# Performance work log

Hardware: AMD Instinct MI355X
Metric: run time of the kernel (lower is better)

## Reference

```python
import jax, jax.numpy as jnp
import numpy as np

N = 100000
E = 1600000
D_IN = 128
H = 128


def _param(key, shape, scale=0.05):
    return jax.random.normal(key, shape, dtype=jnp.float32) * scale


def setup_inputs() -> dict:
    key = jax.random.key(0)
    ks = jax.random.split(key, 24)
    inp = {
        'x': jax.random.normal(ks[0], (N, D_IN), dtype=jnp.float32),
        'edge_index': jax.random.randint(ks[1], (2, E), 0, N, dtype=jnp.int64),
        'h1': jax.random.normal(ks[2], (N, H), dtype=jnp.float32),
        'h2': jax.random.normal(ks[3], (N, H), dtype=jnp.float32),
        'h3': jax.random.normal(ks[4], (N, H), dtype=jnp.float32),
        # GCNConv params (PyG: lin weight applied as x @ W, W: [in, out] here)
        'gcn1_w': _param(ks[5], (D_IN, H)),
        'gcn1_b': jnp.zeros((H,), jnp.float32),
        'gcn2_w': _param(ks[6], (H, H)),
        'gcn2_b': jnp.zeros((H,), jnp.float32),
    }
    # torch.nn.GRUCell params: weight_ih [3H, in], weight_hh [3H, H], biases [3H]
    for i, kw in zip((1, 2, 3), (ks[7], ks[10], ks[13])):
        k1, k2, k3 = jax.random.split(kw, 3)
        inp[f'gru{i}_wih'] = _param(k1, (3 * H, H))
        inp[f'gru{i}_whh'] = _param(k2, (3 * H, H))
        inp[f'gru{i}_bih'] = _param(k3, (3 * H,))
        inp[f'gru{i}_bhh'] = jnp.zeros((3 * H,), jnp.float32)
    return inp


def gcn_conv(x, src, dst, w, b):
    """PyG GCNConv: D^-1/2 (A+I) D^-1/2 X W + b (symmetric norm, self-loops)."""
    xw = x @ w  # [N, H]
    ones = jnp.ones((src.shape[0],), xw.dtype)
    # degree including self-loop
    deg = jax.ops.segment_sum(ones, dst, num_segments=N) + 1.0
    dinv = jax.lax.rsqrt(deg)
    norm = dinv[src] * dinv[dst]  # [E]
    agg = jax.ops.segment_sum(xw[src] * norm[:, None], dst, num_segments=N)
    # self-loop contribution: norm = dinv[i]*dinv[i] = 1/deg[i]
    return agg + xw / deg[:, None] + b


def gru_cell(x, h, w_ih, w_hh, b_ih, b_hh):
    gi = x @ w_ih.T + b_ih  # [N, 3H]
    gh = h @ w_hh.T + b_hh
    i_r, i_z, i_n = jnp.split(gi, 3, axis=-1)
    h_r, h_z, h_n = jnp.split(gh, 3, axis=-1)
    r = jax.nn.sigmoid(i_r + h_r)
    z = jax.nn.sigmoid(i_z + h_z)
    n = jnp.tanh(i_n + r * h_n)
    return (1.0 - z) * n + z * h


def reference(x, edge_index, h1, h2, h3,
              gcn1_w, gcn1_b, gcn2_w, gcn2_b,
              gru1_wih, gru1_whh, gru1_bih, gru1_bhh,
              gru2_wih, gru2_whh, gru2_bih, gru2_bhh,
              gru3_wih, gru3_whh, gru3_bih, gru3_bhh):
    src, dst = edge_index[0], edge_index[1]
    x = jax.nn.relu(gcn_conv(x, src, dst, gcn1_w, gcn1_b))
    # dropout is identity at eval
    x = jax.nn.relu(gcn_conv(x, src, dst, gcn2_w, gcn2_b))
    h1n = gru_cell(x, h1, gru1_wih, gru1_whh, gru1_bih, gru1_bhh)
    h2n = gru_cell(h1n, h2, gru2_wih, gru2_whh, gru2_bih, gru2_bhh)
    h3n = gru_cell(h2n, h3, gru3_wih, gru3_whh, gru3_bih, gru3_bhh)
    return (h1n, h2n, h3n)
```

## Files before the change

### kernel.cpp

```cpp
#include <hip/hip_runtime.h>
#include <hip/hip_bf16.h>

#define DH 128
#define SCB 1024
#define NCHUNK 256
#define LROW 136

typedef __attribute__((ext_vector_type(8))) short short8_t;
typedef __attribute__((ext_vector_type(4))) float f32x4;

static __device__ __forceinline__ short f2bf(float f) {
    union { float f; unsigned u; } v; v.f = f;
    unsigned r = v.u + 0x7fffu + ((v.u >> 16) & 1u);
    return (short)(r >> 16);
}

static __device__ __forceinline__ float bf2f(unsigned short b) {
    union { unsigned u; float f; } v; v.u = ((unsigned)b) << 16;
    return v.f;
}

static __device__ __forceinline__ short8_t cvt8(const float* p) {
    float4 a0 = *(const float4*)p;
    float4 a1 = *(const float4*)(p + 4);
    short8_t t;
    t[0] = f2bf(a0.x); t[1] = f2bf(a0.y); t[2] = f2bf(a0.z); t[3] = f2bf(a0.w);
    t[4] = f2bf(a1.x); t[5] = f2bf(a1.y); t[6] = f2bf(a1.z); t[7] = f2bf(a1.w);
    return t;
}

static __device__ __forceinline__ float sigm(float x) {
    return __builtin_amdgcn_rcpf(1.f + __expf(-x));
}
static __device__ __forceinline__ float tanh_f(float x) {
    return 1.f - 2.f * __builtin_amdgcn_rcpf(__expf(2.f * x) + 1.f);
}

__global__ __launch_bounds__(256) void deg2_k(const int* __restrict__ ei, int E,
                                              unsigned* __restrict__ cnt, int span, int chunkE) {
    int r = blockIdx.x & 7;
    int c = blockIdx.x >> 3;
    int lo = r * span, hi = lo + span;
    long long e0 = (long long)c * chunkE;
    long long e1 = e0 + chunkE; if (e1 > E) e1 = E;
    for (long long e = e0 + threadIdx.x; e < e1; e += 256) {
        int d = ei[E + e];
        if (d >= lo && d < hi) atomicAdd(&cnt[d], 1u);
    }
}

__global__ __launch_bounds__(256) void scan1_k(const unsigned* __restrict__ cnt, int N,
                                               int* __restrict__ offs, unsigned* __restrict__ bsum) {
    __shared__ unsigned s[256];
    int t = threadIdx.x;
    int i0 = blockIdx.x * SCB + t * 4;
    unsigned v0 = (i0 + 0 < N) ? cnt[i0 + 0] : 0u;
    unsigned v1 = (i0 + 1 < N) ? cnt[i0 + 1] : 0u;
    unsigned v2 = (i0 + 2 < N) ? cnt[i0 + 2] : 0u;
    unsigned v3 = (i0 + 3 < N) ? cnt[i0 + 3] : 0u;
    unsigned ts = v0 + v1 + v2 + v3;
    s[t] = ts;
    __syncthreads();
    for (int off = 1; off < 256; off <<= 1) {
        unsigned u = (t >= off) ? s[t - off] : 0u;
        __syncthreads();
        s[t] += u;
        __syncthreads();
    }
    unsigned ex = s[t] - ts;
    if (i0 + 0 < N) offs[i0 + 0] = (int)ex;
    if (i0 + 1 < N) offs[i0 + 1] = (int)(ex + v0);
    if (i0 + 2 < N) offs[i0 + 2] = (int)(ex + v0 + v1);
    if (i0 + 3 < N) offs[i0 + 3] = (int)(ex + v0 + v1 + v2);
    if (t == 255) bsum[blockIdx.x] = s[255];
}

__global__ __launch_bounds__(1024) void scan2_k(unsigned* __restrict__ bsum, int B) {
    __shared__ unsigned s[1024];
    int t = threadIdx.x;
    unsigned v = (t < B) ? bsum[t] : 0u;
    s[t] = v;
    __syncthreads();
    for (int off = 1; off < 1024; off <<= 1) {
        unsigned u = (t >= off) ? s[t - off] : 0u;
        __syncthreads();
        s[t] += u;
        __syncthreads();
    }
    if (t < B) bsum[t] = s[t] - v;
    if (t == 0) bsum[B] = s[1023];
}

__global__ void scan3_k(int* __restrict__ offs, int* __restrict__ cur,
                        float* __restrict__ dinv, const unsigned* __restrict__ cnt,
                        const unsigned* __restrict__ bsum, int N, int B) {
    int i = blockIdx.x * 256 + threadIdx.x;
    if (i < N) {
        int v = offs[i] + (int)bsum[i >> 10];
        offs[i] = v;
        cur[i] = v;
        dinv[i] = rsqrtf((float)cnt[i] + 1.0f);
    }
    if (i == 0) offs[N] = (int)bsum[B];
}

__global__ __launch_bounds__(256) void fill2_k(const int* __restrict__ ei, int E,
                                               int* __restrict__ cur, int* __restrict__ csr_src,
                                               int span, int chunkE) {
    int r = blockIdx.x & 7;
    int c = blockIdx.x >> 3;
    int lo = r * span, hi = lo + span;
    long long e0 = (long long)c * chunkE;
    long long e1 = e0 + chunkE; if (e1 > E) e1 = E;
    for (long long e = e0 + threadIdx.x; e < e1; e += 256) {
        int d = ei[E + e];
        if (d >= lo && d < hi) {
            int pos = atomicAdd(&cur[d], 1);
            csr_src[pos] = ei[e];
        }
    }
}

__global__ void f2bf6_k(const float* __restrict__ s0, const float* __restrict__ s1,
                        const float* __restrict__ s2, const float* __restrict__ s3,
                        const float* __restrict__ s4, const float* __restrict__ s5,
                        short* __restrict__ dst, int WN) {
    int i = blockIdx.x * 256 + threadIdx.x;
    if (i >= 6 * WN) return;
    int b = i / WN, r = i - b * WN;
    const float* srcs[6] = {s0, s1, s2, s3, s4, s5};
    dst[i] = f2bf(srcs[b][r]);
}

__global__ void transpose_bf2_k(const float* __restrict__ sa, const float* __restrict__ sb,
                                short* __restrict__ da, short* __restrict__ db) {
    int i = blockIdx.x * 256 + threadIdx.x;
    int m = i >> 14;
    int j = i & 16383;
    int c = j >> 7, k = j & 127;
    const float* s = m ? sb : sa;
    short* d = m ? db : da;
    d[j] = f2bf(s[k * DH + c]);
}

__global__ __launch_bounds__(256, 4) void gemm_mfma_k(const float* __restrict__ A,
                                                      const short* __restrict__ Wt,
                                                      const float* __restrict__ dinv,
                                                      short* __restrict__ C, int N) {
    int tid = threadIdx.x;
    int wave = tid >> 6, lane = tid & 63;
    int lr = lane & 15, kg = lane >> 4;

    int row0 = blockIdx.x * 128 + wave * 32;
    int ar0 = min(row0 + lr, N - 1);
    int ar1 = min(row0 + 16 + lr, N - 1);
    const float* a0p = A + (size_t)ar0 * DH;
    const float* a1p = A + (size_t)ar1 * DH;
    short8_t af[2][4];
#pragma unroll
    for (int ks = 0; ks < 4; ks++) {
        af[0][ks] = cvt8(a0p + ks * 32 + kg * 8);
        af[1][ks] = cvt8(a1p + ks * 32 + kg * 8);
    }

    float di0[4], di1[4];
#pragma unroll
    for (int j = 0; j < 4; j++) {
        di0[j] = dinv[min(row0 + kg * 4 + j, N - 1)];
        di1[j] = dinv[min(row0 + 16 + kg * 4 + j, N - 1)];
    }

    short8_t bt[3][4];
#define GLOADW(slot, t) { \
    const short* wp = Wt + (size_t)((t) * 16 + lr) * DH + kg * 8; \
    bt[slot][0] = *(const short8_t*)(wp); \
    bt[slot][1] = *(const short8_t*)(wp + 32); \
    bt[slot][2] = *(const short8_t*)(wp + 64); \
    bt[slot][3] = *(const short8_t*)(wp + 96); }

    GLOADW(0, 0)
    GLOADW(1, 1)
#pragma unroll
    for (int t = 0; t < 8; t++) {
        if (t < 6) GLOADW((t + 2) % 3, t + 2)
        f32x4 acc0 = {0.f, 0.f, 0.f, 0.f};
        f32x4 acc1 = {0.f, 0.f, 0.f, 0.f};
#pragma unroll
        for (int ks = 0; ks < 4; ks++) {
            acc0 = __builtin_amdgcn_mfma_f32_16x16x32_bf16(af[0][ks], bt[t % 3][ks], acc0, 0, 0, 0);
            acc1 = __builtin_amdgcn_mfma_f32_16x16x32_bf16(af[1][ks], bt[t % 3][ks], acc1, 0, 0, 0);
        }
        int col = t * 16 + lr;
#pragma unroll
        for (int j = 0; j < 4; j++) {
            int g0 = row0 + kg * 4 + j;
            int g1 = row0 + 16 + kg * 4 + j;
            if (g0 < N) C[(size_t)g0 * DH + col] = f2bf(acc0[j] * di0[j]);
            if (g1 < N) C[(size_t)g1 * DH + col] = f2bf(acc1[j] * di1[j]);
        }
    }
#undef GLOADW
}

__global__ __launch_bounds__(256) void gather_k(const int* __restrict__ csr_src,
                                                const int* __restrict__ offs,
                                                const float* __restrict__ dinv,
                                                const unsigned* __restrict__ xws,
                                                const float* __restrict__ bias,
                                                float* __restrict__ dest, int N) {
    int wid = blockIdx.x * 4 + (threadIdx.x >> 6);
    if (wid >= N) return;
    int lane = threadIdx.x & 63;
    int j = offs[wid];
    int end = offs[wid + 1];
    float dd = dinv[wid];

    unsigned xv = xws[(size_t)wid * 64 + lane];
    float ax = bf2f((unsigned short)(xv & 0xffffu));
    float ay = bf2f((unsigned short)(xv >> 16));

#define ACC(w) { ax += bf2f((unsigned short)((w) & 0xffffu)); \
                 ay += bf2f((unsigned short)((w) >> 16)); }

    if (j + 4 <= end) {
        int a0 = csr_src[j], a1 = csr_src[j + 1], a2 = csr_src[j + 2], a3 = csr_src[j + 3];
        j += 4;
        for (; j + 4 <= end; j += 4) {
            unsigned w0 = xws[(size_t)a0 * 64 + lane];
            unsigned w1 = xws[(size_t)a1 * 64 + lane];
            unsigned w2 = xws[(size_t)a2 * 64 + lane];
            unsigned w3 = xws[(size_t)a3 * 64 + lane];
            a0 = csr_src[j]; a1 = csr_src[j + 1]; a2 = csr_src[j + 2]; a3 = csr_src[j + 3];
            ACC(w0) ACC(w1) ACC(w2) ACC(w3)
        }
        unsigned w0 = xws[(size_t)a0 * 64 + lane];
        unsigned w1 = xws[(size_t)a1 * 64 + lane];
        unsigned w2 = xws[(size_t)a2 * 64 + lane];
        unsigned w3 = xws[(size_t)a3 * 64 + lane];
        ACC(w0) ACC(w1) ACC(w2) ACC(w3)
    }
    for (; j < end; ++j) {
        unsigned w = xws[(size_t)csr_src[j] * 64 + lane];
        ACC(w)
    }
#undef ACC

    float2 b2 = ((const float2*)bias)[lane];
    float ox = fmaxf(fmaf(dd, ax, b2.x), 0.f);
    float oy = fmaxf(fmaf(dd, ay, b2.y), 0.f);
    float2 o; o.x = ox; o.y = oy;
    ((float2*)dest)[(size_t)wid * 64 + lane] = o;
}

__global__ __launch_bounds__(512, 1) void gru3_mfma_k(
        const float* __restrict__ X, const float* __restrict__ H1,
        const float* __restrict__ H2, const float* __restrict__ H3,
        const short* __restrict__ w1i, const short* __restrict__ w1h,
        const short* __restrict__ w2i, const short* __restrict__ w2h,
        const short* __restrict__ w3i, const short* __restrict__ w3h,
        const float* __restrict__ bi1, const float* __restrict__ bh1,
        const float* __restrict__ bi2, const float* __restrict__ bh2,
        const float* __restrict__ bi3, const float* __restrict__ bh3,
        float* __restrict__ o1, float* __restrict__ o2, float* __restrict__ o3,
        int N) {
    __shared__ short lds[4][64 * LROW];
    int tid = threadIdx.x;
    int row0 = blockIdx.x * 64;
    int wave = tid >> 6, lane = tid & 63;
    int lr = lane & 15, kg = lane >> 4;
    int c0 = wave * 16;

    const short* wihs[3] = {w1i, w2i, w3i};
    const short* whhs[3] = {w1h, w2h, w3h};
    const float* bihs[3] = {bi1, bi2, bi3};
    const float* bhhs[3] = {bh1, bh2, bh3};
    float* outs[3] = {o1, o2, o3};

    short8_t bw[3][4], bu[3][4];
#define WLOADALL(wih_, whh_) { \
    _Pragma("unroll") \
    for (int g = 0; g < 3; g++) { \
        const short* wi = (wih_) + (size_t)(g * DH + c0 + lr) * DH + kg * 8; \
        const short* wh = (whh_) + (size_t)(g * DH + c0 + lr) * DH + kg * 8; \
        _Pragma("unroll") \
        for (int ks = 0; ks < 4; ks++) { \
            bw[g][ks] = *(const short8_t*)(wi + ks * 32); \
            bu[g][ks] = *(const short8_t*)(wh + ks * 32); \
        } \
    } }

    {
        const float* mats[4] = {X, H1, H2, H3};
        int mat = tid >> 7;
        int rr = (tid & 127) >> 1;
        int q = tid & 1;
        int grow = min(row0 + rr, N - 1);
        const float* src = mats[mat] + (size_t)grow * DH + q * 64;
        char* dst = (char*)&lds[mat][rr * LROW] + q * 128;
#pragma unroll
        for (int j = 0; j < 8; j++) {
            short8_t v = cvt8(src + j * 8);
            *(short8_t*)(dst + j * 16) = v;
        }
    }
    WLOADALL(w1i, w1h)
    __syncthreads();

    int gcol = c0 + lr;
    int colb = gcol * 2;

#pragma unroll
    for (int cell = 0; cell < 3; cell++) {
        const short* hslot = lds[cell + 1];
        f32x4 aR[4], aZ[4], aI[4], aH[4];
#pragma unroll
        for (int rt = 0; rt < 4; rt++) {
            aR[rt] = (f32x4){0,0,0,0}; aZ[rt] = (f32x4){0,0,0,0};
            aI[rt] = (f32x4){0,0,0,0}; aH[rt] = (f32x4){0,0,0,0};
        }
#pragma unroll
        for (int rt = 0; rt < 4; rt++) {
            int r = rt * 16 + lr;
            const char* xrow = (const char*)&lds[0][r * LROW];
            const char* hrow = (const char*)&hslot[r * LROW];
            short8_t xa[4], ha[4];
#pragma unroll
            for (int ks = 0; ks < 4; ks++) {
                int boff = ks * 64 + kg * 16;
                xa[ks] = *(const short8_t*)(xrow + boff);
                ha[ks] = *(const short8_t*)(hrow + boff);
            }
#pragma unroll
            for (int ks = 0; ks < 4; ks++) {
                aR[rt] = __builtin_amdgcn_mfma_f32_16x16x32_bf16(xa[ks], bw[0][ks], aR[rt], 0, 0, 0);
                aR[rt] = __builtin_amdgcn_mfma_f32_16x16x32_bf16(ha[ks], bu[0][ks], aR[rt], 0, 0, 0);
                aZ[rt] = __builtin_amdgcn_mfma_f32_16x16x32_bf16(xa[ks], bw[1][ks], aZ[rt], 0, 0, 0);
                aZ[rt] = __builtin_amdgcn_mfma_f32_16x16x32_bf16(ha[ks], bu[1][ks], aZ[rt], 0, 0, 0);
                aI[rt] = __builtin_amdgcn_mfma_f32_16x16x32_bf16(xa[ks], bw[2][ks], aI[rt], 0, 0, 0);
                aH[rt] = __builtin_amdgcn_mfma_f32_16x16x32_bf16(ha[ks], bu[2][ks], aH[rt], 0, 0, 0);
            }
        }

        const float* bih = bihs[cell];
        const float* bhh = bhhs[cell];
        float br = bih[gcol], bz = bih[DH + gcol], bn = bih[2 * DH + gcol];
        float cr = bhh[gcol], cz = bhh[DH + gcol], cn = bhh[2 * DH + gcol];
        float* outp = outs[cell];
        short hb[4][4];
#pragma unroll
        for (int rt = 0; rt < 4; rt++) {
#pragma unroll
            for (int j = 0; j < 4; j++) {
                int r = rt * 16 + kg * 4 + j;
                float hv = bf2f(*(const unsigned short*)((const char*)&hslot[r * LROW] + colb));
                float rr = sigm(aR[rt][j] + br + cr);
                float zz = sigm(aZ[rt][j] + bz + cz);
                float nn = tanh_f(aI[rt][j] + bn + rr * (aH[rt][j] + cn));
                float ov = (1.f - zz) * nn + zz * hv;
                int grow = row0 + r;
                if (grow < N) outp[(size_t)grow * DH + gcol] = ov;
                hb[rt][j] = f2bf(ov);
            }
        }

        if (cell < 2) {
            WLOADALL(wihs[cell + 1], whhs[cell + 1])
        }

        __syncthreads();

        if (cell < 2) {
#pragma unroll
            for (int rt = 0; rt < 4; rt++) {
#pragma unroll
                for (int j = 0; j < 4; j++) {
                    int r = rt * 16 + kg * 4 + j;
                    *(short*)((char*)&lds[0][r * LROW] + colb) = hb[rt][j];
                }
            }
            __syncthreads();
        }
    }
#undef WLOADALL
}

extern "C" void kernel_launch(void* const* d_in, const int* in_sizes, int n_in,
                              void* d_out, int out_size, void* d_ws, size_t ws_size,
                              hipStream_t stream) {
    const float* x    = (const float*)d_in[0];
    const int*   ei   = (const int*)d_in[1];
    const float* h1   = (const float*)d_in[2];
    const float* h2   = (const float*)d_in[3];
    const float* h3   = (const float*)d_in[4];
    const float* g1w  = (const float*)d_in[5];
    const float* g1b  = (const float*)d_in[6];
    const float* g2w  = (const float*)d_in[7];
    const float* g2b  = (const float*)d_in[8];
    const float* wih1 = (const float*)d_in[9];
    const float* whh1 = (const float*)d_in[10];
    const float* bih1 = (const float*)d_in[11];
    const float* bhh1 = (const float*)d_in[12];
    const float* wih2 = (const float*)d_in[13];
    const float* whh2 = (const float*)d_in[14];
    const float* bih2 = (const float*)d_in[15];
    const float* bhh2 = (const float*)d_in[16];
    const float* wih3 = (const float*)d_in[17];
    const float* whh3 = (const float*)d_in[18];
    const float* bih3 = (const float*)d_in[19];
    const float* bhh3 = (const float*)d_in[20];

    int N = in_sizes[0] / DH;
    int E = in_sizes[1] / 2;
    int B = (N + SCB - 1) / SCB;
    int nstripes = (N + 127) / 128;
    int nblk64 = (N + 63) / 64;
    int span = (N + 7) / 8;
    int chunkE = (E + NCHUNK - 1) / NCHUNK;

    char* wsp = (char*)d_ws;
    auto alloc = [&](size_t bytes) -> char* {
        char* p = wsp;
        wsp += (bytes + 63) & ~(size_t)63;
        return p;
    };
    unsigned* cnt = (unsigned*)alloc((size_t)N * 4);
    int* offs     = (int*)alloc(((size_t)N + 1) * 4);
    int* cur      = (int*)alloc((size_t)N * 4);
    float* dinv   = (float*)alloc((size_t)N * 4);
    unsigned* bsum= (unsigned*)alloc(((size_t)B + 1) * 4);
    int* csr_src  = (int*)alloc((size_t)E * 4);
    short* xwb    = (short*)alloc((size_t)N * DH * 2);
    float* x2     = (float*)alloc((size_t)N * DH * 4);
    short* w1t    = (short*)alloc((size_t)DH * DH * 2);
    short* w2t    = (short*)alloc((size_t)DH * DH * 2);
    const int WN = 3 * DH * DH;
    short* wbAll  = (short*)alloc((size_t)6 * WN * 2);
    short* wb[6];
    for (int i = 0; i < 6; i++) wb[i] = wbAll + (size_t)i * WN;

    float* out  = (float*)d_out;
    float* h1n  = out;
    float* h2n  = out + (size_t)N * DH;
    float* h3n  = out + 2 * (size_t)N * DH;

    f2bf6_k<<<(6 * WN + 255) / 256, 256, 0, stream>>>(wih1, whh1, wih2, whh2, wih3, whh3, wbAll, WN);
    transpose_bf2_k<<<(2 * DH * DH + 255) / 256, 256, 0, stream>>>(g1w, g2w, w1t, w2t);

    hipMemsetAsync(cnt, 0, (size_t)N * 4, stream);
    deg2_k<<<8 * NCHUNK, 256, 0, stream>>>(ei, E, cnt, span, chunkE);
    scan1_k<<<B, 256, 0, stream>>>(cnt, N, offs, bsum);
    scan2_k<<<1, 1024, 0, stream>>>(bsum, B);
    scan3_k<<<(N + 255) / 256, 256, 0, stream>>>(offs, cur, dinv, cnt, bsum, N, B);
    fill2_k<<<8 * NCHUNK, 256, 0, stream>>>(ei, E, cur, csr_src, span, chunkE);

    int gblocks = (N + 3) / 4;

    gemm_mfma_k<<<nstripes, 256, 0, stream>>>(x, w1t, dinv, xwb, N);
    gather_k<<<gblocks, 256, 0, stream>>>(csr_src, offs, dinv, (const unsigned*)xwb, g1b, x2, N);

    gemm_mfma_k<<<nstripes, 256, 0, stream>>>(x2, w2t, dinv, xwb, N);
    gather_k<<<gblocks, 256, 0, stream>>>(csr_src, offs, dinv, (const unsigned*)xwb, g2b, x2, N);

    gru3_mfma_k<<<nblk64, 512, 0, stream>>>(x2, h1, h2, h3,
                                            wb[0], wb[1], wb[2], wb[3], wb[4], wb[5],
                                            bih1, bhh1, bih2, bhh2, bih3, bhh3,
                                            h1n, h2n, h3n, N);
}
```

Baseline: 589.4 us.

## Store GCN intermediate features as FP8 and stream GRU hidden states per cell

The scaled XW features written by the GEMM are now encoded in a software e4m3-style FP8 format instead of bf16, which halves the bytes the edge-gather kernel pulls per neighbor. The gather decodes the FP8 values in software before accumulating. Separately, the GRU kernel shrinks its LDS from four to two tiles and loads the next cell's hidden state (H2/H3) from global memory while the current cell computes, which should raise occupancy. The FP8 path loses a lot of precision on the aggregated features and adds decode ALU work per element.

```diff
diff --git a/kernel.cpp b/kernel.cpp
--- a/kernel.cpp
+++ b/kernel.cpp
@@ -20,9 +20,40 @@
     return v.f;
 }
 
+static __device__ __forceinline__ unsigned char fp8enc(float f) {
+    union { float f; unsigned u; } v; v.f = f;
+    unsigned s = v.u >> 31;
+    unsigned mag = v.u & 0x7fffffffu;
+    if (mag >= 0x43E00000u) return (unsigned char)((s << 7) | 0x7E);
+    unsigned e = mag >> 23;
+    if (e < 121u) {
+        int q = (int)rintf(fabsf(f) * 512.0f);
+        return (unsigned char)((s << 7) | (unsigned)q);
+    }
+    unsigned r = mag + 0x7FFFFu + ((mag >> 20) & 1u);
+    unsigned e2 = r >> 23, m2 = (r >> 20) & 7u;
+    if (e2 > 135u || (e2 == 135u && m2 == 7u)) return (unsigned char)((s << 7) | 0x7E);
+    return (unsigned char)((s << 7) | ((e2 - 120u) << 3) | m2);
+}
+
+static __device__ __forceinline__ float fp8dec(unsigned b) {
+    unsigned s = b >> 7, E = (b >> 3) & 0xFu, m = b & 7u;
+    union { unsigned u; float f; } v;
+    v.u = (s << 31) | ((E + 120u) << 23) | (m << 20);
+    float sub = (s ? -1.953125e-3f : 1.953125e-3f) * (float)m;
+    return E ? v.f : sub;
+}
+
 static __device__ __forceinline__ short8_t cvt8(const float* p) {
     float4 a0 = *(const float4*)p;
     float4 a1 = *(const float4*)(p + 4);
+    short8_t t;
+    t[0] = f2bf(a0.x); t[1] = f2bf(a0.y); t[2] = f2bf(a0.z); t[3] = f2bf(a0.w);
+    t[4] = f2bf(a1.x); t[5] = f2bf(a1.y); t[6] = f2bf(a1.z); t[7] = f2bf(a1.w);
+    return t;
+}
+
+static __device__ __forceinline__ short8_t cvt8v(float4 a0, float4 a1) {
     short8_t t;
     t[0] = f2bf(a0.x); t[1] = f2bf(a0.y); t[2] = f2bf(a0.z); t[3] = f2bf(a0.w);
     t[4] = f2bf(a1.x); t[5] = f2bf(a1.y); t[6] = f2bf(a1.z); t[7] = f2bf(a1.w);
@@ -146,7 +177,7 @@
 __global__ __launch_bounds__(256, 4) void gemm_mfma_k(const float* __restrict__ A,
                                                       const short* __restrict__ Wt,
                                                       const float* __restrict__ dinv,
-                                                      short* __restrict__ C, int N) {
+                                                      unsigned char* __restrict__ C, int N) {
     int tid = threadIdx.x;
     int wave = tid >> 6, lane = tid & 63;
     int lr = lane & 15, kg = lane >> 4;
@@ -195,8 +226,8 @@
         for (int j = 0; j < 4; j++) {
             int g0 = row0 + kg * 4 + j;
             int g1 = row0 + 16 + kg * 4 + j;
-            if (g0 < N) C[(size_t)g0 * DH + col] = f2bf(acc0[j] * di0[j]);
-            if (g1 < N) C[(size_t)g1 * DH + col] = f2bf(acc1[j] * di1[j]);
+            if (g0 < N) C[(size_t)g0 * DH + col] = fp8enc(acc0[j] * di0[j]);
+            if (g1 < N) C[(size_t)g1 * DH + col] = fp8enc(acc1[j] * di1[j]);
         }
     }
 #undef GLOADW
@@ -205,7 +236,7 @@
 __global__ __launch_bounds__(256) void gather_k(const int* __restrict__ csr_src,
                                                 const int* __restrict__ offs,
                                                 const float* __restrict__ dinv,
-                                                const unsigned* __restrict__ xws,
+                                                const unsigned short* __restrict__ xq2,
                                                 const float* __restrict__ bias,
                                                 float* __restrict__ dest, int N) {
     int wid = blockIdx.x * 4 + (threadIdx.x >> 6);
@@ -215,32 +246,31 @@
     int end = offs[wid + 1];
     float dd = dinv[wid];
 
-    unsigned xv = xws[(size_t)wid * 64 + lane];
-    float ax = bf2f((unsigned short)(xv & 0xffffu));
-    float ay = bf2f((unsigned short)(xv >> 16));
-
-#define ACC(w) { ax += bf2f((unsigned short)((w) & 0xffffu)); \
-                 ay += bf2f((unsigned short)((w) >> 16)); }
+    unsigned xv = xq2[(size_t)wid * 64 + lane];
+    float ax = fp8dec(xv & 0xffu);
+    float ay = fp8dec(xv >> 8);
+
+#define ACC(w) { ax += fp8dec((w) & 0xffu); ay += fp8dec((w) >> 8); }
 
     if (j + 4 <= end) {
         int a0 = csr_src[j], a1 = csr_src[j + 1], a2 = csr_src[j + 2], a3 = csr_src[j + 3];
         j += 4;
         for (; j + 4 <= end; j += 4) {
-            unsigned w0 = xws[(size_t)a0 * 64 + lane];
-            unsigned w1 = xws[(size_t)a1 * 64 + lane];
-            unsigned w2 = xws[(size_t)a2 * 64 + lane];
-            unsigned w3 = xws[(size_t)a3 * 64 + lane];
+            unsigned w0 = xq2[(size_t)a0 * 64 + lane];
+            unsigned w1 = xq2[(size_t)a1 * 64 + lane];
+            unsigned w2 = xq2[(size_t)a2 * 64 + lane];
+            unsigned w3 = xq2[(size_t)a3 * 64 + lane];
             a0 = csr_src[j]; a1 = csr_src[j + 1]; a2 = csr_src[j + 2]; a3 = csr_src[j + 3];
             ACC(w0) ACC(w1) ACC(w2) ACC(w3)
         }
-        unsigned w0 = xws[(size_t)a0 * 64 + lane];
-        unsigned w1 = xws[(size_t)a1 * 64 + lane];
-        unsigned w2 = xws[(size_t)a2 * 64 + lane];
-        unsigned w3 = xws[(size_t)a3 * 64 + lane];
+        unsigned w0 = xq2[(size_t)a0 * 64 + lane];
+        unsigned w1 = xq2[(size_t)a1 * 64 + lane];
+        unsigned w2 = xq2[(size_t)a2 * 64 + lane];
+        unsigned w3 = xq2[(size_t)a3 * 64 + lane];
         ACC(w0) ACC(w1) ACC(w2) ACC(w3)
     }
     for (; j < end; ++j) {
-        unsigned w = xws[(size_t)csr_src[j] * 64 + lane];
+        unsigned w = xq2[(size_t)csr_src[j] * 64 + lane];
         ACC(w)
     }
 #undef ACC
@@ -263,7 +293,7 @@
         const float* __restrict__ bi3, const float* __restrict__ bh3,
         float* __restrict__ o1, float* __restrict__ o2, float* __restrict__ o3,
         int N) {
-    __shared__ short lds[4][64 * LROW];
+    __shared__ short lds[2][64 * LROW];
     int tid = threadIdx.x;
     int row0 = blockIdx.x * 64;
     int wave = tid >> 6, lane = tid & 63;
@@ -289,29 +319,30 @@
         } \
     } }
 
+    WLOADALL(w1i, w1h)
+
     {
-        const float* mats[4] = {X, H1, H2, H3};
-        int mat = tid >> 7;
-        int rr = (tid & 127) >> 1;
-        int q = tid & 1;
-        int grow = min(row0 + rr, N - 1);
-        const float* src = mats[mat] + (size_t)grow * DH + q * 64;
-        char* dst = (char*)&lds[mat][rr * LROW] + q * 128;
-#pragma unroll
-        for (int j = 0; j < 8; j++) {
+        int mat = tid >> 8;
+        int r = (tid & 255) >> 2;
+        int q = tid & 3;
+        int grow = min(row0 + r, N - 1);
+        const float* src = (mat ? H1 : X) + (size_t)grow * DH + q * 32;
+        char* dst = (char*)&lds[mat][r * LROW] + q * 64;
+#pragma unroll
+        for (int j = 0; j < 4; j++) {
             short8_t v = cvt8(src + j * 8);
             *(short8_t*)(dst + j * 16) = v;
         }
     }
-    WLOADALL(w1i, w1h)
     __syncthreads();
 
     int gcol = c0 + lr;
     int colb = gcol * 2;
+    int srow = tid >> 3;
+    int sq = tid & 7;
 
 #pragma unroll
     for (int cell = 0; cell < 3; cell++) {
-        const short* hslot = lds[cell + 1];
         f32x4 aR[4], aZ[4], aI[4], aH[4];
 #pragma unroll
         for (int rt = 0; rt < 4; rt++) {
@@ -322,7 +353,7 @@
         for (int rt = 0; rt < 4; rt++) {
             int r = rt * 16 + lr;
             const char* xrow = (const char*)&lds[0][r * LROW];
-            const char* hrow = (const char*)&hslot[r * LROW];
+            const char* hrow = (const char*)&lds[1][r * LROW];
             short8_t xa[4], ha[4];
 #pragma unroll
             for (int ks = 0; ks < 4; ks++) {
@@ -341,6 +372,16 @@
             }
         }
 
+        float4 hs0, hs1, hs2, hs3;
+        if (cell < 2) {
+            int grow = min(row0 + srow, N - 1);
+            const float* src = (cell == 0 ? H2 : H3) + (size_t)grow * DH + sq * 16;
+            hs0 = *(const float4*)(src + 0);
+            hs1 = *(const float4*)(src + 4);
+            hs2 = *(const float4*)(src + 8);
+            hs3 = *(const float4*)(src + 12);
+        }
+
         const float* bih = bihs[cell];
         const float* bhh = bhhs[cell];
         float br = bih[gcol], bz = bih[DH + gcol], bn = bih[2 * DH + gcol];
@@ -352,7 +393,7 @@
 #pragma unroll
             for (int j = 0; j < 4; j++) {
                 int r = rt * 16 + kg * 4 + j;
-                float hv = bf2f(*(const unsigned short*)((const char*)&hslot[r * LROW] + colb));
+                float hv = bf2f(*(const unsigned short*)((const char*)&lds[1][r * LROW] + colb));
                 float rr = sigm(aR[rt][j] + br + cr);
                 float zz = sigm(aZ[rt][j] + bz + cz);
                 float nn = tanh_f(aI[rt][j] + bn + rr * (aH[rt][j] + cn));
@@ -377,6 +418,11 @@
                     int r = rt * 16 + kg * 4 + j;
                     *(short*)((char*)&lds[0][r * LROW] + colb) = hb[rt][j];
                 }
+            }
+            {
+                char* dst = (char*)&lds[1][srow * LROW] + sq * 32;
+                *(short8_t*)(dst) = cvt8v(hs0, hs1);
+                *(short8_t*)(dst + 16) = cvt8v(hs2, hs3);
             }
             __syncthreads();
         }
@@ -429,7 +475,7 @@
     float* dinv   = (float*)alloc((size_t)N * 4);
     unsigned* bsum= (unsigned*)alloc(((size_t)B + 1) * 4);
     int* csr_src  = (int*)alloc((size_t)E * 4);
-    short* xwb    = (short*)alloc((size_t)N * DH * 2);
+    unsigned char* xq = (unsigned char*)alloc((size_t)N * DH);
     float* x2     = (float*)alloc((size_t)N * DH * 4);
     short* w1t    = (short*)alloc((size_t)DH * DH * 2);
     short* w2t    = (short*)alloc((size_t)DH * DH * 2);
@@ -455,11 +501,11 @@
 
     int gblocks = (N + 3) / 4;
 
-    gemm_mfma_k<<<nstripes, 256, 0, stream>>>(x, w1t, dinv, xwb, N);
-    gather_k<<<gblocks, 256, 0, stream>>>(csr_src, offs, dinv, (const unsigned*)xwb, g1b, x2, N);
-
-    gemm_mfma_k<<<nstripes, 256, 0, stream>>>(x2, w2t, dinv, xwb, N);
-    gather_k<<<gblocks, 256, 0, stream>>>(csr_src, offs, dinv, (const unsigned*)xwb, g2b, x2, N);
+    gemm_mfma_k<<<nstripes, 256, 0, stream>>>(x, w1t, dinv, xq, N);
+    gather_k<<<gblocks, 256, 0, stream>>>(csr_src, offs, dinv, (const unsigned short*)xq, g1b, x2, N);
+
+    gemm_mfma_k<<<nstripes, 256, 0, stream>>>(x2, w2t, dinv, xq, N);
+    gather_k<<<gblocks, 256, 0, stream>>>(csr_src, offs, dinv, (const unsigned short*)xq, g2b, x2, N);
 
     gru3_mfma_k<<<nblk64, 512, 0, stream>>>(x2, h1, h2, h3,
                                             wb[0], wb[1], wb[2], wb[3], wb[4], wb[5],
```

Result: slower. 658.5 us (+11.7%).

## Halve GRU LDS footprint and prefetch next hidden state during current cell

Applied to the files above, without the earlier changes.

The fused three-cell GRU kernel now keeps only two LDS slots (input and current hidden) instead of four. H2 and H3 are loaded from global memory into registers while the current cell's epilogue runs, then converted to bf16 and written into the hidden slot after the barrier. Weight loads for the first cell are also issued before the initial tile staging. This cuts LDS use per block, which could allow more blocks per CU, and overlaps hidden-state loads with compute, at the cost of extra registers and less parallelism in the initial load.

```diff
diff --git a/kernel.cpp b/kernel.cpp
--- a/kernel.cpp
+++ b/kernel.cpp
@@ -23,6 +23,13 @@
 static __device__ __forceinline__ short8_t cvt8(const float* p) {
     float4 a0 = *(const float4*)p;
     float4 a1 = *(const float4*)(p + 4);
+    short8_t t;
+    t[0] = f2bf(a0.x); t[1] = f2bf(a0.y); t[2] = f2bf(a0.z); t[3] = f2bf(a0.w);
+    t[4] = f2bf(a1.x); t[5] = f2bf(a1.y); t[6] = f2bf(a1.z); t[7] = f2bf(a1.w);
+    return t;
+}
+
+static __device__ __forceinline__ short8_t cvt8v(float4 a0, float4 a1) {
     short8_t t;
     t[0] = f2bf(a0.x); t[1] = f2bf(a0.y); t[2] = f2bf(a0.z); t[3] = f2bf(a0.w);
     t[4] = f2bf(a1.x); t[5] = f2bf(a1.y); t[6] = f2bf(a1.z); t[7] = f2bf(a1.w);
@@ -263,7 +270,7 @@
         const float* __restrict__ bi3, const float* __restrict__ bh3,
         float* __restrict__ o1, float* __restrict__ o2, float* __restrict__ o3,
         int N) {
-    __shared__ short lds[4][64 * LROW];
+    __shared__ short lds[2][64 * LROW];
     int tid = threadIdx.x;
     int row0 = blockIdx.x * 64;
     int wave = tid >> 6, lane = tid & 63;
@@ -289,29 +296,30 @@
         } \
     } }
 
+    WLOADALL(w1i, w1h)
+
     {
-        const float* mats[4] = {X, H1, H2, H3};
-        int mat = tid >> 7;
-        int rr = (tid & 127) >> 1;
-        int q = tid & 1;
-        int grow = min(row0 + rr, N - 1);
-        const float* src = mats[mat] + (size_t)grow * DH + q * 64;
-        char* dst = (char*)&lds[mat][rr * LROW] + q * 128;
-#pragma unroll
-        for (int j = 0; j < 8; j++) {
+        int mat = tid >> 8;
+        int r = (tid & 255) >> 2;
+        int q = tid & 3;
+        int grow = min(row0 + r, N - 1);
+        const float* src = (mat ? H1 : X) + (size_t)grow * DH + q * 32;
+        char* dst = (char*)&lds[mat][r * LROW] + q * 64;
+#pragma unroll
+        for (int j = 0; j < 4; j++) {
             short8_t v = cvt8(src + j * 8);
             *(short8_t*)(dst + j * 16) = v;
         }
     }
-    WLOADALL(w1i, w1h)
     __syncthreads();
 
     int gcol = c0 + lr;
     int colb = gcol * 2;
+    int srow = tid >> 3;
+    int sq = tid & 7;
 
 #pragma unroll
     for (int cell = 0; cell < 3; cell++) {
-        const short* hslot = lds[cell + 1];
         f32x4 aR[4], aZ[4], aI[4], aH[4];
 #pragma unroll
         for (int rt = 0; rt < 4; rt++) {
@@ -322,7 +330,7 @@
         for (int rt = 0; rt < 4; rt++) {
             int r = rt * 16 + lr;
             const char* xrow = (const char*)&lds[0][r * LROW];
-            const char* hrow = (const char*)&hslot[r * LROW];
+            const char* hrow = (const char*)&lds[1][r * LROW];
             short8_t xa[4], ha[4];
 #pragma unroll
             for (int ks = 0; ks < 4; ks++) {
@@ -341,6 +349,16 @@
             }
         }
 
+        float4 hs0, hs1, hs2, hs3;
+        if (cell < 2) {
+            int grow = min(row0 + srow, N - 1);
+            const float* src = (cell == 0 ? H2 : H3) + (size_t)grow * DH + sq * 16;
+            hs0 = *(const float4*)(src + 0);
+            hs1 = *(const float4*)(src + 4);
+            hs2 = *(const float4*)(src + 8);
+            hs3 = *(const float4*)(src + 12);
+        }
+
         const float* bih = bihs[cell];
         const float* bhh = bhhs[cell];
         float br = bih[gcol], bz = bih[DH + gcol], bn = bih[2 * DH + gcol];
@@ -352,7 +370,7 @@
 #pragma unroll
             for (int j = 0; j < 4; j++) {
                 int r = rt * 16 + kg * 4 + j;
-                float hv = bf2f(*(const unsigned short*)((const char*)&hslot[r * LROW] + colb));
+                float hv = bf2f(*(const unsigned short*)((const char*)&lds[1][r * LROW] + colb));
                 float rr = sigm(aR[rt][j] + br + cr);
                 float zz = sigm(aZ[rt][j] + bz + cz);
                 float nn = tanh_f(aI[rt][j] + bn + rr * (aH[rt][j] + cn));
@@ -377,6 +395,11 @@
                     int r = rt * 16 + kg * 4 + j;
                     *(short*)((char*)&lds[0][r * LROW] + colb) = hb[rt][j];
                 }
+            }
+            {
+                char* dst = (char*)&lds[1][srow * LROW] + sq * 32;
+                *(short8_t*)(dst) = cvt8v(hs0, hs1);
+                *(short8_t*)(dst + 16) = cvt8v(hs2, hs3);
             }
             __syncthreads();
         }
```

Measured after the change: 554.7 us. 5.9% less time.
